# Kernel tuning notes

Hardware: AMD Instinct MI355X
Metric: run time of the kernel (lower is better)

## Reference

```python
import jax, jax.numpy as jnp
import numpy as np

QMAX = 127.0
EPS = 1e-12


def _smooth_quant(x, col_scale):
    """Per-row int8 quantization of (x * col_scale).
    Returns (q, row_scale): q holds integer values in [-127, 127] (kept in f32,
    exactly representable), row_scale is abs-max/127 per row."""
    xs = x * col_scale                                  # [R, K]
    row_scale = jnp.max(jnp.abs(xs), axis=-1) / QMAX    # [R]
    row_scale = jnp.maximum(row_scale, EPS)
    q = jnp.clip(jnp.round(xs / row_scale[:, None]), -QMAX, QMAX)
    return q, row_scale


def setup_inputs() -> dict:
    key = jax.random.key(0)
    k1, k2, k3 = jax.random.split(key, 3)
    B, S, K, N = 4, 8192, 1024, 1024
    input_ = jax.random.normal(k1, (B, S, K), dtype=jnp.float32)
    weight = jax.random.normal(k2, (N, K), dtype=jnp.float32) * 0.02
    bias = jax.random.normal(k3, (N,), dtype=jnp.float32) * 0.01
    return {"input": input_, "weight": weight, "bias": bias}


def reference(input, weight, bias):
    x2 = input.reshape(-1, input.shape[-1])             # [M, K]
    # SmoothQuant smoothing scale: sqrt(colmax(|x|) * colmax(|w|)), shape [K]
    in_max = jnp.max(jnp.abs(x2), axis=0)
    w_max = jnp.max(jnp.abs(weight), axis=0)
    smooth_scale = jnp.sqrt(jnp.maximum(in_max * w_max, EPS))
    # quantize activations divided by smooth_scale, weights multiplied by it
    x_q, x_s = _smooth_quant(x2, 1.0 / smooth_scale)    # [M,K], [M]
    w_q, w_s = _smooth_quant(weight, smooth_scale)      # [N,K], [N]
    # int8 matmul (emulated exactly in f32) + row/col dequant scales + bias
    acc = x_q @ w_q.T                                   # [M, N]
    out = acc * x_s[:, None] * w_s[None, :] + bias
    return out.reshape(*input.shape[:-1], weight.shape[0])
```

## Files before the change

### kernel.cpp

```cpp
#include <hip/hip_runtime.h>


typedef int v4i __attribute__((ext_vector_type(4)));

__device__ __forceinline__ void gld_lds16(const void* g, void* l) {
    __builtin_amdgcn_global_load_lds(
        (const __attribute__((address_space(1))) void*)g,
        (__attribute__((address_space(3))) void*)l,
        16, 0, 0);
}

__global__ __launch_bounds__(256) void colmax_part_kernel(const float* __restrict__ src,
                                                          int rows, int rpb, int K,
                                                          float* __restrict__ partial) {
    const int c = threadIdx.x * 4;
    int r0 = blockIdx.x * rpb;
    int r1 = r0 + rpb; if (r1 > rows) r1 = rows;
    float m0 = 0.f, m1 = 0.f, m2 = 0.f, m3 = 0.f;
    const float* p = src + (size_t)r0 * K + c;
#pragma unroll 8
    for (int r = r0; r < r1; ++r, p += K) {
        float4 v = *(const float4*)p;
        m0 = fmaxf(m0, fabsf(v.x));
        m1 = fmaxf(m1, fabsf(v.y));
        m2 = fmaxf(m2, fabsf(v.z));
        m3 = fmaxf(m3, fabsf(v.w));
    }
    float4 o; o.x = m0; o.y = m1; o.z = m2; o.w = m3;
    *(float4*)(partial + (size_t)blockIdx.x * K + c) = o;
}

__global__ void finalize_kernel(const float* __restrict__ px, int nx,
                                const float* __restrict__ pw, int nw,
                                float* __restrict__ smooth, float* __restrict__ inv_s, int K) {
    int c = blockIdx.x * blockDim.x + threadIdx.x;
    if (c >= K) return;
    float mx = 0.f, mw = 0.f;
    for (int r = 0; r < nx; ++r) mx = fmaxf(mx, px[(size_t)r * K + c]);
    for (int r = 0; r < nw; ++r) mw = fmaxf(mw, pw[(size_t)r * K + c]);
    float s = sqrtf(fmaxf(mx * mw, 1e-12f));
    smooth[c] = s;
    inv_s[c]  = 1.0f / s;
}

__global__ __launch_bounds__(256) void quant_rows_wave_kernel(
    const float* __restrict__ src, const float* __restrict__ colscale,
    signed char* __restrict__ q, float* __restrict__ rowscale, int K) {
    const int wave = threadIdx.x >> 6, lane = threadIdx.x & 63;
    const int row = blockIdx.x * 4 + wave;
    const float* srow = src + (size_t)row * K + lane * 16;
    const float* crow = colscale + lane * 16;
    float xs[16];
    float mv = 0.f;
#pragma unroll
    for (int i = 0; i < 4; ++i) {
        float4 v  = *(const float4*)(srow + i * 4);
        float4 cs = *(const float4*)(crow + i * 4);
        xs[i*4+0] = v.x * cs.x; xs[i*4+1] = v.y * cs.y;
        xs[i*4+2] = v.z * cs.z; xs[i*4+3] = v.w * cs.w;
        mv = fmaxf(mv, fmaxf(fmaxf(fabsf(xs[i*4+0]), fabsf(xs[i*4+1])),
                             fmaxf(fabsf(xs[i*4+2]), fabsf(xs[i*4+3]))));
    }
#pragma unroll
    for (int off = 32; off > 0; off >>= 1)
        mv = fmaxf(mv, __shfl_xor(mv, off, 64));
    const float rs = fmaxf(mv / 127.0f, 1e-12f);
    unsigned pk[4];
#pragma unroll
    for (int i = 0; i < 4; ++i) {
        float q0 = fminf(fmaxf(rintf(xs[i*4+0] / rs), -127.f), 127.f);
        float q1 = fminf(fmaxf(rintf(xs[i*4+1] / rs), -127.f), 127.f);
        float q2 = fminf(fmaxf(rintf(xs[i*4+2] / rs), -127.f), 127.f);
        float q3 = fminf(fmaxf(rintf(xs[i*4+3] / rs), -127.f), 127.f);
        int b0 = (int)q0, b1 = (int)q1, b2 = (int)q2, b3 = (int)q3;
        pk[i] = (unsigned)(b0 & 0xff) | ((unsigned)(b1 & 0xff) << 8)
              | ((unsigned)(b2 & 0xff) << 16) | ((unsigned)(b3 & 0xff) << 24);
    }
    *(uint4*)(q + (size_t)row * K + lane * 16) = make_uint4(pk[0], pk[1], pk[2], pk[3]);
    if (lane == 0) rowscale[row] = rs;
}

__global__ __launch_bounds__(512, 2) void gemm_i8_kernel(
    const signed char* __restrict__ Aq,
    const signed char* __restrict__ Bq,
    const float* __restrict__ xs,
    const float* __restrict__ wsc,
    const float* __restrict__ bias,
    float* __restrict__ out,
    int M, int N, int K) {
    __shared__ __align__(16) signed char As[65536];
    __shared__ __align__(16) signed char Bs[65536];

    const int tid  = threadIdx.x;
    const int lane = tid & 63;
    const int wave = tid >> 6;
    const int wm = wave >> 2;
    const int wn = wave & 3;
    const int g  = lane >> 4;
    const int fr = lane & 15;

    const int NT = K >> 7;

    const int nwg = gridDim.x;
    const int wg  = (blockIdx.x & 7) * (nwg >> 3) + (blockIdx.x >> 3);
    const int nTn = N >> 8;
    const int tm = wg / nTn, tn = wg % nTn;
    const int bm = tm << 8, bn = tn << 8;

    const int srow = tid >> 2;
    const int schk = (tid & 3) ^ (srow & 3);
    const signed char* srcA0 = Aq + (size_t)(bm + srow) * K + schk * 16;
    const signed char* srcA1 = srcA0 + (size_t)128 * K;
    const signed char* srcB0 = Bq + (size_t)(bn + srow) * K + schk * 16;
    const signed char* srcB1 = srcB0 + (size_t)128 * K;
    const int ldsSt = tid * 16;

    const int swz   = (g ^ (fr & 3)) * 16;
    const int aBase = (wm * 128 + fr) * 64 + swz;
    const int bBase = (wn * 64 + fr) * 64 + swz;

    v4i acc[8][4] = {};
    v4i bf[4];

#define STAGE_A(T, KS) do { \
        const int go_ = (T) * 128 + (KS) * 64; \
        signed char* l_ = &As[((T) & 1) * 32768 + (KS) * 16384 + ldsSt]; \
        gld_lds16(srcA0 + go_, l_); \
        gld_lds16(srcA1 + go_, l_ + 8192); \
    } while (0)
#define STAGE_B(T, KS) do { \
        const int go_ = (T) * 128 + (KS) * 64; \
        signed char* l_ = &Bs[((T) & 1) * 32768 + (KS) * 16384 + ldsSt]; \
        gld_lds16(srcB0 + go_, l_); \
        gld_lds16(srcB1 + go_, l_ + 8192); \
    } while (0)

#define PHASE(BUF, KS, MH, STG, WAIT) \
    do { \
        const int hb_ = (BUF) * 32768 + (KS) * 16384; \
        v4i af[4]; \
        _Pragma("unroll") \
        for (int i = 0; i < 4; ++i) \
            af[i] = *(const v4i*)&As[hb_ + aBase + ((MH) * 4 + i) * 1024]; \
        if ((MH) == 0) { \
            _Pragma("unroll") \
            for (int j = 0; j < 4; ++j) \
                bf[j] = *(const v4i*)&Bs[hb_ + bBase + j * 1024]; \
        } \
        STG; \
        asm volatile("s_waitcnt " WAIT ::: "memory"); \
        asm volatile("s_barrier" ::: "memory"); \
        asm volatile("s_waitcnt lgkmcnt(0)" ::: "memory"); \
        __builtin_amdgcn_sched_barrier(0); \
        __builtin_amdgcn_s_setprio(1); \
        _Pragma("unroll") \
        for (int i = 0; i < 4; ++i) \
            _Pragma("unroll") \
            for (int j = 0; j < 4; ++j) \
                acc[(MH) * 4 + i][j] = __builtin_amdgcn_mfma_i32_16x16x64_i8( \
                    af[i], bf[j], acc[(MH) * 4 + i][j], 0, 0, 0); \
        __builtin_amdgcn_s_setprio(0); \
        asm volatile("s_barrier" ::: "memory"); \
    } while (0)

    STAGE_A(0, 0); STAGE_B(0, 0);
    STAGE_A(0, 1); STAGE_B(0, 1);
    STAGE_A(1, 0); STAGE_B(1, 0);
    asm volatile("s_waitcnt vmcnt(4)" ::: "memory");
    asm volatile("s_barrier" ::: "memory");

    for (int t = 0; t < NT - 2; ++t) {
        const int buf = t & 1;
        PHASE(buf, 0, 0, STAGE_A(t + 1, 1), "vmcnt(8)");
        PHASE(buf, 0, 1, STAGE_B(t + 1, 1), "vmcnt(8)");
        PHASE(buf, 1, 0, STAGE_A(t + 2, 0), "vmcnt(8)");
        PHASE(buf, 1, 1, STAGE_B(t + 2, 0), "vmcnt(8)");
    }
    {
        const int t = NT - 2, buf = t & 1;
        PHASE(buf, 0, 0, STAGE_A(t + 1, 1), "vmcnt(8)");
        PHASE(buf, 0, 1, STAGE_B(t + 1, 1), "vmcnt(8)");
        PHASE(buf, 1, 0, (void)0, "vmcnt(8)");
        PHASE(buf, 1, 1, (void)0, "vmcnt(4)");
    }
    {
        const int buf = (NT - 1) & 1;
        PHASE(buf, 0, 0, (void)0, "vmcnt(4)");
        PHASE(buf, 0, 1, (void)0, "vmcnt(0)");
        PHASE(buf, 1, 0, (void)0, "vmcnt(0)");
        PHASE(buf, 1, 1, (void)0, "vmcnt(0)");
    }
#undef PHASE
#undef STAGE_A
#undef STAGE_B

    const int orow0 = bm + wm * 128 + g * 4;
    const int ocol0 = bn + wn * 64 + fr;
    float wv[4], bvv[4];
#pragma unroll
    for (int j = 0; j < 4; ++j) {
        wv[j]  = wsc[ocol0 + j * 16];
        bvv[j] = bias[ocol0 + j * 16];
    }
#pragma unroll
    for (int i = 0; i < 8; ++i) {
#pragma unroll
        for (int r = 0; r < 4; ++r) {
            const int row = orow0 + i * 16 + r;
            const float xv = xs[row];
            float* op = out + (size_t)row * N + ocol0;
#pragma unroll
            for (int j = 0; j < 4; ++j)
                op[j * 16] = (float)acc[i][j][r] * xv * wv[j] + bvv[j];
        }
    }
}

extern "C" void kernel_launch(void* const* d_in, const int* in_sizes, int n_in,
                              void* d_out, int out_size, void* d_ws, size_t ws_size,
                              hipStream_t stream) {
    const float* x    = (const float*)d_in[0];
    const float* w    = (const float*)d_in[1];
    const float* bias = (const float*)d_in[2];
    float* out = (float*)d_out;

    const int N = in_sizes[2];
    const int K = in_sizes[1] / N;
    const int M = in_sizes[0] / K;

    char* ws = (char*)d_ws;
    float* p1x       = (float*)(ws);
    float* p2x       = (float*)(ws + 4194304);
    float* pw        = (float*)(ws + 4259840);
    float* smooth    = (float*)(ws + 4325376);
    float* inv_s     = (float*)(ws + 4329472);
    float* w_s       = (float*)(ws + 4333568);
    float* x_s       = (float*)(ws + 4337664);
    signed char* x_q = (signed char*)(ws + 4468736);
    signed char* w_q = x_q + (size_t)M * K;

    colmax_part_kernel<<<1024, 256, 0, stream>>>(x, M, 32, K, p1x);
    colmax_part_kernel<<<16, 256, 0, stream>>>(p1x, 1024, 64, K, p2x);
    colmax_part_kernel<<<16, 256, 0, stream>>>(w, N, 64, K, pw);
    finalize_kernel<<<(K + 255) / 256, 256, 0, stream>>>(p2x, 16, pw, 16, smooth, inv_s, K);
    quant_rows_wave_kernel<<<N / 4, 256, 0, stream>>>(w, smooth, w_q, w_s, K);
    quant_rows_wave_kernel<<<M / 4, 256, 0, stream>>>(x, inv_s, x_q, x_s, K);
    gemm_i8_kernel<<<(M / 256) * (N / 256), 512, 0, stream>>>(x_q, w_q, x_s, w_s, bias, out, M, N, K);
}
```

Baseline: 317.5 us.

## Shrink GEMM tile to 128x128 and fuse small reduction and quant launches

The int8 GEMM moves from 256x256 tiles with 512 threads to 128x128 tiles with 256 threads. LDS per block and accumulator registers are halved, and the grid grows fourfold, which should raise occupancy and improve load balance across CUs, at the cost of reloading A and B more often. The second-stage column-max reductions for x and w are merged into one launch, as are the weight and activation quantization kernels. The first colmax pass now uses 512 blocks of 64 rows, which cuts launch overhead and the size of the partial buffer.

```diff
diff --git a/kernel.cpp b/kernel.cpp
--- a/kernel.cpp
+++ b/kernel.cpp
@@ -10,12 +10,10 @@
         16, 0, 0);
 }
 
-__global__ __launch_bounds__(256) void colmax_part_kernel(const float* __restrict__ src,
-                                                          int rows, int rpb, int K,
-                                                          float* __restrict__ partial) {
+__device__ __forceinline__ void colmax_body(const float* __restrict__ src,
+                                            int r0, int r1, int K,
+                                            float* __restrict__ dst) {
     const int c = threadIdx.x * 4;
-    int r0 = blockIdx.x * rpb;
-    int r1 = r0 + rpb; if (r1 > rows) r1 = rows;
     float m0 = 0.f, m1 = 0.f, m2 = 0.f, m3 = 0.f;
     const float* p = src + (size_t)r0 * K + c;
 #pragma unroll 8
@@ -27,7 +25,29 @@
         m3 = fmaxf(m3, fabsf(v.w));
     }
     float4 o; o.x = m0; o.y = m1; o.z = m2; o.w = m3;
-    *(float4*)(partial + (size_t)blockIdx.x * K + c) = o;
+    *(float4*)(dst + c) = o;
+}
+
+__global__ __launch_bounds__(256) void colmax_part_kernel(const float* __restrict__ src,
+                                                          int rows, int rpb, int K,
+                                                          float* __restrict__ partial) {
+    int r0 = blockIdx.x * rpb;
+    int r1 = r0 + rpb; if (r1 > rows) r1 = rows;
+    colmax_body(src, r0, r1, K, partial + (size_t)blockIdx.x * K);
+}
+
+__global__ __launch_bounds__(256) void part2_fused_kernel(const float* __restrict__ p1x, int nx,
+                                                          const float* __restrict__ w, int nw,
+                                                          float* __restrict__ p2x,
+                                                          float* __restrict__ pw, int K) {
+    const int b = blockIdx.x;
+    if (b < 16) {
+        const int rpb = nx >> 4;
+        colmax_body(p1x, b * rpb, (b + 1) * rpb, K, p2x + (size_t)b * K);
+    } else {
+        const int rpb = nw >> 4;
+        colmax_body(w, (b - 16) * rpb, (b - 15) * rpb, K, pw + (size_t)(b - 16) * K);
+    }
 }
 
 __global__ void finalize_kernel(const float* __restrict__ px, int nx,
@@ -43,11 +63,11 @@
     inv_s[c]  = 1.0f / s;
 }
 
-__global__ __launch_bounds__(256) void quant_rows_wave_kernel(
-    const float* __restrict__ src, const float* __restrict__ colscale,
-    signed char* __restrict__ q, float* __restrict__ rowscale, int K) {
-    const int wave = threadIdx.x >> 6, lane = threadIdx.x & 63;
-    const int row = blockIdx.x * 4 + wave;
+__device__ __forceinline__ void quant_row_body(const float* __restrict__ src,
+                                               const float* __restrict__ colscale,
+                                               signed char* __restrict__ q,
+                                               float* __restrict__ rowscale,
+                                               int row, int K, int lane) {
     const float* srow = src + (size_t)row * K + lane * 16;
     const float* crow = colscale + lane * 16;
     float xs[16];
@@ -80,7 +100,22 @@
     if (lane == 0) rowscale[row] = rs;
 }
 
-__global__ __launch_bounds__(512, 2) void gemm_i8_kernel(
+__global__ __launch_bounds__(256) void quant_fused_kernel(
+    const float* __restrict__ w, const float* __restrict__ x,
+    const float* __restrict__ smooth, const float* __restrict__ inv_s,
+    signed char* __restrict__ w_q, float* __restrict__ w_s,
+    signed char* __restrict__ x_q, float* __restrict__ x_s,
+    int K, int wblocks) {
+    const int wave = threadIdx.x >> 6, lane = threadIdx.x & 63;
+    const int b = blockIdx.x;
+    if (b < wblocks) {
+        quant_row_body(w, smooth, w_q, w_s, b * 4 + wave, K, lane);
+    } else {
+        quant_row_body(x, inv_s, x_q, x_s, (b - wblocks) * 4 + wave, K, lane);
+    }
+}
+
+__global__ __launch_bounds__(256, 2) void gemm_i8_kernel(
     const signed char* __restrict__ Aq,
     const signed char* __restrict__ Bq,
     const float* __restrict__ xs,
@@ -88,14 +123,14 @@
     const float* __restrict__ bias,
     float* __restrict__ out,
     int M, int N, int K) {
-    __shared__ __align__(16) signed char As[65536];
-    __shared__ __align__(16) signed char Bs[65536];
+    __shared__ __align__(16) signed char As[32768];
+    __shared__ __align__(16) signed char Bs[32768];
 
     const int tid  = threadIdx.x;
     const int lane = tid & 63;
     const int wave = tid >> 6;
-    const int wm = wave >> 2;
-    const int wn = wave & 3;
+    const int wm = wave >> 1;
+    const int wn = wave & 1;
     const int g  = lane >> 4;
     const int fr = lane & 15;
 
@@ -103,45 +138,45 @@
 
     const int nwg = gridDim.x;
     const int wg  = (blockIdx.x & 7) * (nwg >> 3) + (blockIdx.x >> 3);
-    const int nTn = N >> 8;
+    const int nTn = N >> 7;
     const int tm = wg / nTn, tn = wg % nTn;
-    const int bm = tm << 8, bn = tn << 8;
+    const int bm = tm << 7, bn = tn << 7;
 
     const int srow = tid >> 2;
     const int schk = (tid & 3) ^ (srow & 3);
     const signed char* srcA0 = Aq + (size_t)(bm + srow) * K + schk * 16;
-    const signed char* srcA1 = srcA0 + (size_t)128 * K;
+    const signed char* srcA1 = srcA0 + (size_t)64 * K;
     const signed char* srcB0 = Bq + (size_t)(bn + srow) * K + schk * 16;
-    const signed char* srcB1 = srcB0 + (size_t)128 * K;
+    const signed char* srcB1 = srcB0 + (size_t)64 * K;
     const int ldsSt = tid * 16;
 
     const int swz   = (g ^ (fr & 3)) * 16;
-    const int aBase = (wm * 128 + fr) * 64 + swz;
+    const int aBase = (wm * 64 + fr) * 64 + swz;
     const int bBase = (wn * 64 + fr) * 64 + swz;
 
-    v4i acc[8][4] = {};
+    v4i acc[4][4] = {};
     v4i bf[4];
 
 #define STAGE_A(T, KS) do { \
         const int go_ = (T) * 128 + (KS) * 64; \
-        signed char* l_ = &As[((T) & 1) * 32768 + (KS) * 16384 + ldsSt]; \
+        signed char* l_ = &As[((T) & 1) * 16384 + (KS) * 8192 + ldsSt]; \
         gld_lds16(srcA0 + go_, l_); \
-        gld_lds16(srcA1 + go_, l_ + 8192); \
+        gld_lds16(srcA1 + go_, l_ + 4096); \
     } while (0)
 #define STAGE_B(T, KS) do { \
         const int go_ = (T) * 128 + (KS) * 64; \
-        signed char* l_ = &Bs[((T) & 1) * 32768 + (KS) * 16384 + ldsSt]; \
+        signed char* l_ = &Bs[((T) & 1) * 16384 + (KS) * 8192 + ldsSt]; \
         gld_lds16(srcB0 + go_, l_); \
-        gld_lds16(srcB1 + go_, l_ + 8192); \
+        gld_lds16(srcB1 + go_, l_ + 4096); \
     } while (0)
 
 #define PHASE(BUF, KS, MH, STG, WAIT) \
     do { \
-        const int hb_ = (BUF) * 32768 + (KS) * 16384; \
-        v4i af[4]; \
+        const int hb_ = (BUF) * 16384 + (KS) * 8192; \
+        v4i af[2]; \
         _Pragma("unroll") \
-        for (int i = 0; i < 4; ++i) \
-            af[i] = *(const v4i*)&As[hb_ + aBase + ((MH) * 4 + i) * 1024]; \
+        for (int i = 0; i < 2; ++i) \
+            af[i] = *(const v4i*)&As[hb_ + aBase + ((MH) * 2 + i) * 1024]; \
         if ((MH) == 0) { \
             _Pragma("unroll") \
             for (int j = 0; j < 4; ++j) \
@@ -154,11 +189,11 @@
         __builtin_amdgcn_sched_barrier(0); \
         __builtin_amdgcn_s_setprio(1); \
         _Pragma("unroll") \
-        for (int i = 0; i < 4; ++i) \
+        for (int i = 0; i < 2; ++i) \
             _Pragma("unroll") \
             for (int j = 0; j < 4; ++j) \
-                acc[(MH) * 4 + i][j] = __builtin_amdgcn_mfma_i32_16x16x64_i8( \
-                    af[i], bf[j], acc[(MH) * 4 + i][j], 0, 0, 0); \
+                acc[(MH) * 2 + i][j] = __builtin_amdgcn_mfma_i32_16x16x64_i8( \
+                    af[i], bf[j], acc[(MH) * 2 + i][j], 0, 0, 0); \
         __builtin_amdgcn_s_setprio(0); \
         asm volatile("s_barrier" ::: "memory"); \
     } while (0)
@@ -194,7 +229,7 @@
 #undef STAGE_A
 #undef STAGE_B
 
-    const int orow0 = bm + wm * 128 + g * 4;
+    const int orow0 = bm + wm * 64 + g * 4;
     const int ocol0 = bn + wn * 64 + fr;
     float wv[4], bvv[4];
 #pragma unroll
@@ -203,7 +238,7 @@
         bvv[j] = bias[ocol0 + j * 16];
     }
 #pragma unroll
-    for (int i = 0; i < 8; ++i) {
+    for (int i = 0; i < 4; ++i) {
 #pragma unroll
         for (int r = 0; r < 4; ++r) {
             const int row = orow0 + i * 16 + r;
@@ -230,20 +265,19 @@
 
     char* ws = (char*)d_ws;
     float* p1x       = (float*)(ws);
-    float* p2x       = (float*)(ws + 4194304);
-    float* pw        = (float*)(ws + 4259840);
-    float* smooth    = (float*)(ws + 4325376);
-    float* inv_s     = (float*)(ws + 4329472);
-    float* w_s       = (float*)(ws + 4333568);
-    float* x_s       = (float*)(ws + 4337664);
-    signed char* x_q = (signed char*)(ws + 4468736);
+    float* p2x       = (float*)(ws + 2097152);
+    float* pw        = (float*)(ws + 2162688);
+    float* smooth    = (float*)(ws + 2228224);
+    float* inv_s     = (float*)(ws + 2232320);
+    float* w_s       = (float*)(ws + 2236416);
+    float* x_s       = (float*)(ws + 2240512);
+    signed char* x_q = (signed char*)(ws + 2371584);
     signed char* w_q = x_q + (size_t)M * K;
 
-    colmax_part_kernel<<<1024, 256, 0, stream>>>(x, M, 32, K, p1x);
-    colmax_part_kernel<<<16, 256, 0, stream>>>(p1x, 1024, 64, K, p2x);
-    colmax_part_kernel<<<16, 256, 0, stream>>>(w, N, 64, K, pw);
+    colmax_part_kernel<<<512, 256, 0, stream>>>(x, M, 64, K, p1x);
+    part2_fused_kernel<<<32, 256, 0, stream>>>(p1x, 512, w, N, p2x, pw, K);
     finalize_kernel<<<(K + 255) / 256, 256, 0, stream>>>(p2x, 16, pw, 16, smooth, inv_s, K);
-    quant_rows_wave_kernel<<<N / 4, 256, 0, stream>>>(w, smooth, w_q, w_s, K);
-    quant_rows_wave_kernel<<<M / 4, 256, 0, stream>>>(x, inv_s, x_q, x_s, K);
-    gemm_i8_kernel<<<(M / 256) * (N / 256), 512, 0, stream>>>(x_q, w_q, x_s, w_s, bias, out, M, N, K);
-}
+    quant_fused_kernel<<<N / 4 + M / 4, 256, 0, stream>>>(w, x, smooth, inv_s,
+                                                          w_q, w_s, x_q, x_s, K, N / 4);
+    gemm_i8_kernel<<<(M / 128) * (N / 128), 256, 0, stream>>>(x_q, w_q, x_s, w_s, bias, out, M, N, K);
+}
```

After: 321.3 us. About the same (+1.2%).
